# Optimization experiments

Measured on AMD Instinct MI355X. Metric: run time of the kernel, lower is better.

Reference implementation:

```python
import jax, jax.numpy as jnp
import numpy as np

TEMPERATURE = 0.1
EPS = 1e-12  # torch F.normalize eps


def setup_inputs() -> dict:
    key = jax.random.key(0)
    k1, k2 = jax.random.split(key)
    B, D = 4096, 512
    z_i = jax.random.normal(k1, (B, D), dtype=jnp.float32)
    z_j = jax.random.normal(k2, (B, D), dtype=jnp.float32)
    return {"z_i": z_i, "z_j": z_j}


def reference(z_i, z_j):
    B = z_i.shape[0]
    N = 2 * B
    z = jnp.concatenate([z_i, z_j], axis=0)  # [N, D]
    norm = jnp.linalg.norm(z, axis=1, keepdims=True)
    z = z / jnp.maximum(norm, EPS)
    sim = jnp.matmul(z, z.T) / TEMPERATURE  # [N, N]

    idx = jnp.arange(N)
    neg_inf = jnp.float32(-jnp.inf)
    # mask self-similarity diagonal
    sim = sim.at[idx, idx].set(neg_inf)

    b = jnp.arange(B)
    # positives: diag(sim, +B) then diag(sim, -B)
    positives = jnp.concatenate([sim[b, b + B], sim[b + B, b]]).reshape(N, 1)

    # negatives: sim with positive pairs also masked to -inf
    negatives = sim.at[b, b + B].set(neg_inf)
    negatives = negatives.at[b + B, b].set(neg_inf)

    logits = jnp.concatenate([positives, negatives], axis=1)  # [N, N+1]
    # cross entropy with target class 0 for every row
    lse = jax.scipy.special.logsumexp(logits, axis=1)
    loss = jnp.mean(lse - logits[:, 0])
    return loss
```

## Files before the change

kernel.cpp:

```cpp
#include <hip/hip_runtime.h>
#include <hip/hip_bf16.h>

#define BATCH 4096
#define NTOT  8192
#define DIM   512
#define NBLK  2080

typedef __attribute__((ext_vector_type(4))) float floatx4;

#define ASYNC16(gp, lp)                                                        \
  __builtin_amdgcn_global_load_lds(                                            \
      (__attribute__((address_space(1))) void*)(gp),                           \
      (__attribute__((address_space(3))) void*)(lp), 16, 0, 0)

__global__ __launch_bounds__(256) void nrm_kernel(const float* __restrict__ zi,
                                                  const float* __restrict__ zj,
                                                  unsigned char* __restrict__ zn,
                                                  float* __restrict__ S,
                                                  float* __restrict__ out) {
  if (blockIdx.x < 32) S[blockIdx.x * 256 + threadIdx.x] = 0.0f;
  if (blockIdx.x == 32 && threadIdx.x == 0) out[0] = 0.0f;
  const int row = blockIdx.x * 4 + (threadIdx.x >> 6);
  const int l   = threadIdx.x & 63;
  const float* src = (row < BATCH) ? (zi + (size_t)row * DIM)
                                   : (zj + (size_t)(row - BATCH) * DIM);
  const float4* s4 = (const float4*)src;
  float4 v0 = s4[l];
  float4 v1 = s4[l + 64];
  float ss = v0.x*v0.x + v0.y*v0.y + v0.z*v0.z + v0.w*v0.w
           + v1.x*v1.x + v1.y*v1.y + v1.z*v1.z + v1.w*v1.w;
  #pragma unroll
  for (int m = 1; m < 64; m <<= 1) ss += __shfl_xor(ss, m, 64);
  const float r = 16.0f / fmaxf(sqrtf(ss), 1e-12f);
  int p0 = __builtin_amdgcn_cvt_pk_fp8_f32(v0.x * r, v0.y * r, 0, false);
  p0     = __builtin_amdgcn_cvt_pk_fp8_f32(v0.z * r, v0.w * r, p0, true);
  int p1 = __builtin_amdgcn_cvt_pk_fp8_f32(v1.x * r, v1.y * r, 0, false);
  p1     = __builtin_amdgcn_cvt_pk_fp8_f32(v1.z * r, v1.w * r, p1, true);
  int* d = (int*)(zn + (size_t)row * DIM);
  d[l]       = p0;
  d[l + 64]  = p1;
}

__global__ __launch_bounds__(256) void simsum_kernel(const unsigned char* __restrict__ zn,
                                                     float* __restrict__ S,
                                                     float* __restrict__ P) {
  const int u = blockIdx.x;
  int bj = (int)((sqrtf(8.0f * (float)u + 1.0f) - 1.0f) * 0.5f);
  while ((bj + 1) * (bj + 2) / 2 <= u) ++bj;
  while (bj * (bj + 1) / 2 > u) --bj;
  const int bi = u - bj * (bj + 1) / 2;
  const bool diag = (bi == bj);
  const bool posb = (bj == bi + BATCH / 128);

  __shared__ __align__(16) unsigned char shA[2 * 8192];
  __shared__ __align__(16) unsigned char shB[2 * 8192];
  __shared__ float redR[2][128];
  __shared__ float redC[2][128];

  const int t    = threadIdx.x;
  const int w    = t >> 6;
  const int l    = t & 63;
  const int quad = l >> 4;
  const int lo   = l & 15;
  const int wm   = w >> 1;
  const int wn   = w & 1;
  const int tileRow = bi * 128;
  const int tileCol = bj * 128;

  const int c0 = t;
  const int r0 = c0 >> 2, m0 = c0 & 3;
  const int off0 = ((2 * m0) ^ (r0 & 6)) * 8;
  const unsigned char* gA0 = zn + (size_t)(tileRow + r0) * DIM + off0;
  const unsigned char* gA1 = zn + (size_t)(tileRow + r0 + 64) * DIM + off0;
  const unsigned char* gB0 = zn + (size_t)(tileCol + r0) * DIM + off0;
  const unsigned char* gB1 = zn + (size_t)(tileCol + r0 + 64) * DIM + off0;
  unsigned char* lA0 = shA + w * 1024;
  unsigned char* lA1 = shA + w * 1024 + 4096;
  unsigned char* lB0 = shB + w * 1024;
  unsigned char* lB1 = shB + w * 1024 + 4096;

  floatx4 acc[4][4];
  #pragma unroll
  for (int i = 0; i < 4; ++i)
    #pragma unroll
    for (int j = 0; j < 4; ++j)
      acc[i][j] = (floatx4){0.f, 0.f, 0.f, 0.f};

  const int s0 = ((quad ^ (lo & 6))) * 8;
  const int s1 = s0 ^ 32;
  const int aRow = (wm * 64 + lo) * 64;
  const int bRow = (wn * 64 + lo) * 64;

  ASYNC16(gA0, lA0); ASYNC16(gA1, lA1);
  ASYNC16(gB0, lB0); ASYNC16(gB1, lB1);
  gA0 += 64; gA1 += 64; gB0 += 64; gB1 += 64;

  #pragma unroll
  for (int it = 0; it < 8; ++it) {
    __syncthreads();
    const int co = (it & 1) * 8192;
    const int no = co ^ 8192;
    if (it < 7) {
      ASYNC16(gA0, lA0 + no); ASYNC16(gA1, lA1 + no);
      ASYNC16(gB0, lB0 + no); ASYNC16(gB1, lB1 + no);
      gA0 += 64; gA1 += 64; gB0 += 64; gB1 += 64;
    }
    long a0[4], a1[4], b0[4], b1[4];
    #pragma unroll
    for (int i = 0; i < 4; ++i) {
      a0[i] = *(const long*)(shA + co + aRow + i * 1024 + s0);
      a1[i] = *(const long*)(shA + co + aRow + i * 1024 + s1);
    }
    #pragma unroll
    for (int j = 0; j < 4; ++j) {
      b0[j] = *(const long*)(shB + co + bRow + j * 1024 + s0);
      b1[j] = *(const long*)(shB + co + bRow + j * 1024 + s1);
    }
    #pragma unroll
    for (int i = 0; i < 4; ++i)
      #pragma unroll
      for (int j = 0; j < 4; ++j) {
        acc[i][j] = __builtin_amdgcn_mfma_f32_16x16x32_fp8_fp8(a0[i], b0[j],
                                                               acc[i][j], 0, 0, 0);
        acc[i][j] = __builtin_amdgcn_mfma_f32_16x16x32_fp8_fp8(a1[i], b1[j],
                                                               acc[i][j], 0, 0, 0);
      }
  }

  const float LS = 10.0f / 256.0f;
  float rs[4][4];
  float cs[4];
  #pragma unroll
  for (int i = 0; i < 4; ++i)
    #pragma unroll
    for (int r = 0; r < 4; ++r) rs[i][r] = 0.f;
  #pragma unroll
  for (int j = 0; j < 4; ++j) cs[j] = 0.f;

  #pragma unroll
  for (int i = 0; i < 4; ++i)
    #pragma unroll
    for (int j = 0; j < 4; ++j)
      #pragma unroll
      for (int r = 0; r < 4; ++r) {
        const float e = __expf(acc[i][j][r] * LS - 10.0f);
        rs[i][r] += e;
        cs[j] += e;
      }

  if (wm == wn && quad == (lo >> 2)) {
    const int r = lo & 3;
    if (diag) {
      #pragma unroll
      for (int i = 0; i < 4; ++i) {
        const float e = __expf(acc[i][i][r] * LS - 10.0f);
        rs[i][r] -= e;
        cs[i] -= e;
      }
    }
    if (posb) {
      #pragma unroll
      for (int i = 0; i < 4; ++i) {
        const int row = tileRow + wm * 64 + i * 16 + lo;
        const float v = acc[i][i][r] * LS;
        P[row] = v;
        P[row + BATCH] = v;
      }
    }
  }

  #pragma unroll
  for (int m = 1; m < 16; m <<= 1) {
    #pragma unroll
    for (int i = 0; i < 4; ++i)
      #pragma unroll
      for (int r = 0; r < 4; ++r)
        rs[i][r] += __shfl_xor(rs[i][r], m, 64);
  }
  if (lo == 0) {
    #pragma unroll
    for (int i = 0; i < 4; ++i)
      #pragma unroll
      for (int r = 0; r < 4; ++r)
        redR[wn][wm * 64 + i * 16 + quad * 4 + r] = rs[i][r];
  }
  #pragma unroll
  for (int m = 16; m < 64; m <<= 1) {
    #pragma unroll
    for (int j = 0; j < 4; ++j) cs[j] += __shfl_xor(cs[j], m, 64);
  }
  if (quad == 0) {
    #pragma unroll
    for (int j = 0; j < 4; ++j)
      redC[wm][wn * 64 + j * 16 + lo] = cs[j];
  }
  __syncthreads();
  if (t < 128) {
    atomicAdd(&S[tileRow + t], redR[0][t] + redR[1][t]);
  } else if (!diag) {
    const int c = t - 128;
    atomicAdd(&S[tileCol + c], redC[0][c] + redC[1][c]);
  }
}

__global__ __launch_bounds__(256) void loss_kernel(const float* __restrict__ S,
                                                   const float* __restrict__ P,
                                                   float* __restrict__ out) {
  const int i = blockIdx.x * 256 + threadIdx.x;
  float a = 10.0f + logf(S[i]) - P[i];
  #pragma unroll
  for (int m = 1; m < 64; m <<= 1) a += __shfl_xor(a, m, 64);
  __shared__ float sb[4];
  if ((threadIdx.x & 63) == 0) sb[threadIdx.x >> 6] = a;
  __syncthreads();
  if (threadIdx.x == 0)
    atomicAdd(out, (sb[0] + sb[1] + sb[2] + sb[3]) * (1.0f / (float)NTOT));
}

extern "C" void kernel_launch(void* const* d_in, const int* in_sizes, int n_in,
                              void* d_out, int out_size, void* d_ws, size_t ws_size,
                              hipStream_t stream) {
  const float* zi = (const float*)d_in[0];
  const float* zj = (const float*)d_in[1];
  unsigned char* zn = (unsigned char*)d_ws;
  float*  S  = (float*)((char*)d_ws + (size_t)NTOT * DIM * 2);
  float*  P  = S + NTOT;
  float*  out = (float*)d_out;

  nrm_kernel<<<NTOT / 4, 256, 0, stream>>>(zi, zj, zn, S, out);
  simsum_kernel<<<NBLK, 256, 0, stream>>>(zn, S, P);
  loss_kernel<<<NTOT / 256, 256, 0, stream>>>(S, P, out);
}
```

Before: 101.7 us.

## Use gfx950 scaled 16x16x128 FP8 MFMA with 128-byte K stages

Replaces the pairs of 16x16x32 FP8 MFMAs with the MI355X scaled 16x16x128 f8f6f4 MFMA, using unit scales (exponent 127), so each instruction covers four times the K depth. The K stage grows from 64 to 128 bytes, halving the number of pipeline iterations and barriers. LDS layout, swizzle and async load addressing are reworked to match, with 16-byte fragment reads per lane. This doubles shared memory per block to 64KB, which may reduce occupancy, and relies on the lane-to-K mapping of the new instruction being correct.

```diff
diff --git a/kernel.cpp b/kernel.cpp
--- a/kernel.cpp
+++ b/kernel.cpp
@@ -7,6 +7,7 @@
 #define NBLK  2080
 
 typedef __attribute__((ext_vector_type(4))) float floatx4;
+typedef __attribute__((ext_vector_type(8))) int   intx8;
 
 #define ASYNC16(gp, lp)                                                        \
   __builtin_amdgcn_global_load_lds(                                            \
@@ -52,8 +53,8 @@
   const bool diag = (bi == bj);
   const bool posb = (bj == bi + BATCH / 128);
 
-  __shared__ __align__(16) unsigned char shA[2 * 8192];
-  __shared__ __align__(16) unsigned char shB[2 * 8192];
+  __shared__ __align__(16) unsigned char shA[2 * 16384];
+  __shared__ __align__(16) unsigned char shB[2 * 16384];
   __shared__ float redR[2][128];
   __shared__ float redC[2][128];
 
@@ -67,17 +68,18 @@
   const int tileRow = bi * 128;
   const int tileCol = bj * 128;
 
-  const int c0 = t;
-  const int r0 = c0 >> 2, m0 = c0 & 3;
-  const int off0 = ((2 * m0) ^ (r0 & 6)) * 8;
-  const unsigned char* gA0 = zn + (size_t)(tileRow + r0) * DIM + off0;
-  const unsigned char* gA1 = zn + (size_t)(tileRow + r0 + 64) * DIM + off0;
-  const unsigned char* gB0 = zn + (size_t)(tileCol + r0) * DIM + off0;
-  const unsigned char* gB1 = zn + (size_t)(tileCol + r0 + 64) * DIM + off0;
-  unsigned char* lA0 = shA + w * 1024;
-  unsigned char* lA1 = shA + w * 1024 + 4096;
-  unsigned char* lB0 = shB + w * 1024;
-  unsigned char* lB1 = shB + w * 1024 + 4096;
+  const int rr   = t >> 3;
+  const int koff = ((t & 7) ^ (rr & 7)) * 16;
+  const unsigned char* gA0 = zn + (size_t)(tileRow + rr      ) * DIM + koff;
+  const unsigned char* gA1 = zn + (size_t)(tileRow + rr + 32 ) * DIM + koff;
+  const unsigned char* gA2 = zn + (size_t)(tileRow + rr + 64 ) * DIM + koff;
+  const unsigned char* gA3 = zn + (size_t)(tileRow + rr + 96 ) * DIM + koff;
+  const unsigned char* gB0 = zn + (size_t)(tileCol + rr      ) * DIM + koff;
+  const unsigned char* gB1 = zn + (size_t)(tileCol + rr + 32 ) * DIM + koff;
+  const unsigned char* gB2 = zn + (size_t)(tileCol + rr + 64 ) * DIM + koff;
+  const unsigned char* gB3 = zn + (size_t)(tileCol + rr + 96 ) * DIM + koff;
+  unsigned char* lA = shA + w * 1024;
+  unsigned char* lB = shB + w * 1024;
 
   floatx4 acc[4][4];
   #pragma unroll
@@ -86,46 +88,47 @@
     for (int j = 0; j < 4; ++j)
       acc[i][j] = (floatx4){0.f, 0.f, 0.f, 0.f};
 
-  const int s0 = ((quad ^ (lo & 6))) * 8;
-  const int s1 = s0 ^ 32;
-  const int aRow = (wm * 64 + lo) * 64;
-  const int bRow = (wn * 64 + lo) * 64;
-
-  ASYNC16(gA0, lA0); ASYNC16(gA1, lA1);
-  ASYNC16(gB0, lB0); ASYNC16(gB1, lB1);
-  gA0 += 64; gA1 += 64; gB0 += 64; gB1 += 64;
-
-  #pragma unroll
-  for (int it = 0; it < 8; ++it) {
+  const int s0   = ((2 * quad)     ^ (lo & 7)) * 16;
+  const int s1   = ((2 * quad + 1) ^ (lo & 7)) * 16;
+  const int aRow = (wm * 64 + lo) * 128;
+  const int bRow = (wn * 64 + lo) * 128;
+
+  #define STAGE(bufo)                                                         \
+    ASYNC16(gA0, lA + (bufo));          ASYNC16(gA1, lA + (bufo) + 4096);     \
+    ASYNC16(gA2, lA + (bufo) + 8192);   ASYNC16(gA3, lA + (bufo) + 12288);    \
+    ASYNC16(gB0, lB + (bufo));          ASYNC16(gB1, lB + (bufo) + 4096);     \
+    ASYNC16(gB2, lB + (bufo) + 8192);   ASYNC16(gB3, lB + (bufo) + 12288);    \
+    gA0 += 128; gA1 += 128; gA2 += 128; gA3 += 128;                           \
+    gB0 += 128; gB1 += 128; gB2 += 128; gB3 += 128;
+
+  STAGE(0)
+
+  #pragma unroll
+  for (int it = 0; it < 4; ++it) {
     __syncthreads();
-    const int co = (it & 1) * 8192;
-    const int no = co ^ 8192;
-    if (it < 7) {
-      ASYNC16(gA0, lA0 + no); ASYNC16(gA1, lA1 + no);
-      ASYNC16(gB0, lB0 + no); ASYNC16(gB1, lB1 + no);
-      gA0 += 64; gA1 += 64; gB0 += 64; gB1 += 64;
-    }
-    long a0[4], a1[4], b0[4], b1[4];
+    const int co = (it & 1) * 16384;
+    const int no = co ^ 16384;
+    if (it < 3) { STAGE(no) }
+    union frag { int4 h[2]; intx8 v; };
+    frag aF[4], bF[4];
     #pragma unroll
     for (int i = 0; i < 4; ++i) {
-      a0[i] = *(const long*)(shA + co + aRow + i * 1024 + s0);
-      a1[i] = *(const long*)(shA + co + aRow + i * 1024 + s1);
+      aF[i].h[0] = *(const int4*)(shA + co + aRow + i * 2048 + s0);
+      aF[i].h[1] = *(const int4*)(shA + co + aRow + i * 2048 + s1);
     }
     #pragma unroll
     for (int j = 0; j < 4; ++j) {
-      b0[j] = *(const long*)(shB + co + bRow + j * 1024 + s0);
-      b1[j] = *(const long*)(shB + co + bRow + j * 1024 + s1);
+      bF[j].h[0] = *(const int4*)(shB + co + bRow + j * 2048 + s0);
+      bF[j].h[1] = *(const int4*)(shB + co + bRow + j * 2048 + s1);
     }
     #pragma unroll
     for (int i = 0; i < 4; ++i)
       #pragma unroll
-      for (int j = 0; j < 4; ++j) {
-        acc[i][j] = __builtin_amdgcn_mfma_f32_16x16x32_fp8_fp8(a0[i], b0[j],
-                                                               acc[i][j], 0, 0, 0);
-        acc[i][j] = __builtin_amdgcn_mfma_f32_16x16x32_fp8_fp8(a1[i], b1[j],
-                                                               acc[i][j], 0, 0, 0);
-      }
-  }
+      for (int j = 0; j < 4; ++j)
+        acc[i][j] = __builtin_amdgcn_mfma_scale_f32_16x16x128_f8f6f4(
+            aF[i].v, bF[j].v, acc[i][j], 0, 0, 0, 127, 0, 127);
+  }
+  #undef STAGE
 
   const float LS = 10.0f / 256.0f;
   float rs[4][4];
```

After: 98.80 us. -2.8%, faster.

## Quantize normalized embeddings to FP4 and use scaled 16x16x128 MFMA

Applied to the files above, without the earlier changes.

Replaces the FP8 encoding of the normalized rows with a hand-rolled 4-bit e2m1-style quantizer at a larger pre-scale. This halves the workspace row size to 256 bytes. The similarity kernel now loads 16-byte fragments with a new swizzle and runs four K-iterations of the scaled f8f6f4 MFMA in FP4 mode instead of eight iterations of paired FP8 MFMAs. The logit scale is adjusted to match. This cuts operand traffic, LDS reads and matrix instruction count, but greatly coarsens the similarity values, which risks loss accuracy.

```diff
diff --git a/kernel.cpp b/kernel.cpp
--- a/kernel.cpp
+++ b/kernel.cpp
@@ -7,11 +7,26 @@
 #define NBLK  2080
 
 typedef __attribute__((ext_vector_type(4))) float floatx4;
+typedef __attribute__((ext_vector_type(8))) int   intx8;
 
 #define ASYNC16(gp, lp)                                                        \
   __builtin_amdgcn_global_load_lds(                                            \
       (__attribute__((address_space(1))) void*)(gp),                           \
       (__attribute__((address_space(3))) void*)(lp), 16, 0, 0)
+
+__device__ __forceinline__ unsigned q4(float v) {
+  const float m = fabsf(v);
+  int c;
+  if      (m < 0.25f) c = 0;
+  else if (m < 0.75f) c = 1;
+  else if (m < 1.25f) c = 2;
+  else if (m < 1.75f) c = 3;
+  else if (m < 2.50f) c = 4;
+  else if (m < 3.50f) c = 5;
+  else if (m < 5.00f) c = 6;
+  else                c = 7;
+  return (unsigned)(c | (v < 0.0f ? 8 : 0));
+}
 
 __global__ __launch_bounds__(256) void nrm_kernel(const float* __restrict__ zi,
                                                   const float* __restrict__ zj,
@@ -31,14 +46,14 @@
            + v1.x*v1.x + v1.y*v1.y + v1.z*v1.z + v1.w*v1.w;
   #pragma unroll
   for (int m = 1; m < 64; m <<= 1) ss += __shfl_xor(ss, m, 64);
-  const float r = 16.0f / fmaxf(sqrtf(ss), 1e-12f);
-  int p0 = __builtin_amdgcn_cvt_pk_fp8_f32(v0.x * r, v0.y * r, 0, false);
-  p0     = __builtin_amdgcn_cvt_pk_fp8_f32(v0.z * r, v0.w * r, p0, true);
-  int p1 = __builtin_amdgcn_cvt_pk_fp8_f32(v1.x * r, v1.y * r, 0, false);
-  p1     = __builtin_amdgcn_cvt_pk_fp8_f32(v1.z * r, v1.w * r, p1, true);
-  int* d = (int*)(zn + (size_t)row * DIM);
-  d[l]       = p0;
-  d[l + 64]  = p1;
+  const float r = 64.0f / fmaxf(sqrtf(ss), 1e-12f);
+  unsigned short p0 = (unsigned short)(q4(v0.x * r) | (q4(v0.y * r) << 4)
+                     | (q4(v0.z * r) << 8) | (q4(v0.w * r) << 12));
+  unsigned short p1 = (unsigned short)(q4(v1.x * r) | (q4(v1.y * r) << 4)
+                     | (q4(v1.z * r) << 8) | (q4(v1.w * r) << 12));
+  unsigned short* d = (unsigned short*)(zn + (size_t)row * 256);
+  d[l]      = p0;
+  d[l + 64] = p1;
 }
 
 __global__ __launch_bounds__(256) void simsum_kernel(const unsigned char* __restrict__ zn,
@@ -67,13 +82,12 @@
   const int tileRow = bi * 128;
   const int tileCol = bj * 128;
 
-  const int c0 = t;
-  const int r0 = c0 >> 2, m0 = c0 & 3;
-  const int off0 = ((2 * m0) ^ (r0 & 6)) * 8;
-  const unsigned char* gA0 = zn + (size_t)(tileRow + r0) * DIM + off0;
-  const unsigned char* gA1 = zn + (size_t)(tileRow + r0 + 64) * DIM + off0;
-  const unsigned char* gB0 = zn + (size_t)(tileCol + r0) * DIM + off0;
-  const unsigned char* gB1 = zn + (size_t)(tileCol + r0 + 64) * DIM + off0;
+  const int rr   = t >> 2;
+  const int koff = ((t & 3) ^ (rr & 3) ^ ((rr >> 2) & 3)) * 16;
+  const unsigned char* gA0 = zn + (size_t)(tileRow + rr     ) * 256 + koff;
+  const unsigned char* gA1 = zn + (size_t)(tileRow + rr + 64) * 256 + koff;
+  const unsigned char* gB0 = zn + (size_t)(tileCol + rr     ) * 256 + koff;
+  const unsigned char* gB1 = zn + (size_t)(tileCol + rr + 64) * 256 + koff;
   unsigned char* lA0 = shA + w * 1024;
   unsigned char* lA1 = shA + w * 1024 + 4096;
   unsigned char* lB0 = shB + w * 1024;
@@ -86,48 +100,45 @@
     for (int j = 0; j < 4; ++j)
       acc[i][j] = (floatx4){0.f, 0.f, 0.f, 0.f};
 
-  const int s0 = ((quad ^ (lo & 6))) * 8;
-  const int s1 = s0 ^ 32;
-  const int aRow = (wm * 64 + lo) * 64;
-  const int bRow = (wn * 64 + lo) * 64;
-
-  ASYNC16(gA0, lA0); ASYNC16(gA1, lA1);
-  ASYNC16(gB0, lB0); ASYNC16(gB1, lB1);
-  gA0 += 64; gA1 += 64; gB0 += 64; gB1 += 64;
-
-  #pragma unroll
-  for (int it = 0; it < 8; ++it) {
+  const int sw   = (quad ^ (lo & 3) ^ ((lo >> 2) & 3)) * 16;
+  const int aRow = (wm * 64 + lo) * 64 + sw;
+  const int bRow = (wn * 64 + lo) * 64 + sw;
+
+  #define STAGE(bufo)                                                         \
+    ASYNC16(gA0, lA0 + (bufo)); ASYNC16(gA1, lA1 + (bufo));                   \
+    ASYNC16(gB0, lB0 + (bufo)); ASYNC16(gB1, lB1 + (bufo));                   \
+    gA0 += 64; gA1 += 64; gB0 += 64; gB1 += 64;
+
+  STAGE(0)
+
+  #pragma unroll
+  for (int it = 0; it < 4; ++it) {
     __syncthreads();
     const int co = (it & 1) * 8192;
     const int no = co ^ 8192;
-    if (it < 7) {
-      ASYNC16(gA0, lA0 + no); ASYNC16(gA1, lA1 + no);
-      ASYNC16(gB0, lB0 + no); ASYNC16(gB1, lB1 + no);
-      gA0 += 64; gA1 += 64; gB0 += 64; gB1 += 64;
-    }
-    long a0[4], a1[4], b0[4], b1[4];
+    if (it < 3) { STAGE(no) }
+    union frag { int4 h[2]; intx8 v; };
+    frag aF[4], bF[4];
     #pragma unroll
     for (int i = 0; i < 4; ++i) {
-      a0[i] = *(const long*)(shA + co + aRow + i * 1024 + s0);
-      a1[i] = *(const long*)(shA + co + aRow + i * 1024 + s1);
+      aF[i].h[0] = *(const int4*)(shA + co + aRow + i * 1024);
+      aF[i].h[1] = aF[i].h[0];
     }
     #pragma unroll
     for (int j = 0; j < 4; ++j) {
-      b0[j] = *(const long*)(shB + co + bRow + j * 1024 + s0);
-      b1[j] = *(const long*)(shB + co + bRow + j * 1024 + s1);
+      bF[j].h[0] = *(const int4*)(shB + co + bRow + j * 1024);
+      bF[j].h[1] = bF[j].h[0];
     }
     #pragma unroll
     for (int i = 0; i < 4; ++i)
       #pragma unroll
-      for (int j = 0; j < 4; ++j) {
-        acc[i][j] = __builtin_amdgcn_mfma_f32_16x16x32_fp8_fp8(a0[i], b0[j],
-                                                               acc[i][j], 0, 0, 0);
-        acc[i][j] = __builtin_amdgcn_mfma_f32_16x16x32_fp8_fp8(a1[i], b1[j],
-                                                               acc[i][j], 0, 0, 0);
-      }
-  }
-
-  const float LS = 10.0f / 256.0f;
+      for (int j = 0; j < 4; ++j)
+        acc[i][j] = __builtin_amdgcn_mfma_scale_f32_16x16x128_f8f6f4(
+            aF[i].v, bF[j].v, acc[i][j], 4, 4, 0, 127, 0, 127);
+  }
+  #undef STAGE
+
+  const float LS = 10.0f / 4096.0f;
   float rs[4][4];
   float cs[4];
   #pragma unroll
```

After: 90.06 us (median of 2 runs). 11.4% less time.
